# Performance work log

Hardware: AMD Instinct MI355X
Metric: run time of the kernel (lower is better)

The kernel has to match this reference:

```python
import jax, jax.numpy as jnp
import numpy as np

M, K, N = 8192, 4096, 4096  # tokens, in_features, out_features

def setup_inputs() -> dict:
    key = jax.random.key(0)
    k1, k2, k3 = jax.random.split(key, 3)
    x = jax.random.normal(k1, (M, K), dtype=jnp.float32)
    # kaiming_uniform_(a=sqrt(5)) on [out,in] -> uniform(-1/sqrt(in), 1/sqrt(in))
    bound = 1.0 / np.sqrt(K)
    weight = jax.random.uniform(k2, (N, K), dtype=jnp.float32, minval=-bound, maxval=bound)
    bias = jax.random.uniform(k3, (N,), dtype=jnp.float32, minval=-bound, maxval=bound)
    return {
        "x": x,
        "weight": weight,
        "bias": bias,
        "input_scale": jnp.float32(1.0),
        "weight_scale": jnp.float32(1.0),
    }


def reference(x, weight, bias, input_scale, weight_scale):
    # Quantize input and weight to fp8 e4m3 (per-tensor scale = 1.0 in module),
    # then dequant-matmul: out = (x_fp8 @ w_fp8^T) * scale_a * scale_b + bias,
    # matching torch._scaled_mm semantics with out_dtype=float32.
    x_fp8 = x.astype(jnp.float8_e4m3fn)
    w_fp8 = weight.astype(jnp.float8_e4m3fn)
    out = jnp.einsum(
        "mk,nk->mn",
        x_fp8.astype(jnp.float32),
        w_fp8.astype(jnp.float32),
    ) * (input_scale * weight_scale)
    return out + bias[None, :]
```

## Files before the change

kernel.cpp:

```cpp
#include <hip/hip_runtime.h>
#include <hip/hip_fp8.h>
#include <cstdint>

typedef float f32x4 __attribute__((ext_vector_type(4)));
typedef int i32x8 __attribute__((ext_vector_type(8)));
typedef long long i64;

static constexpr int Mdim = 8192;
static constexpr int Kdim = 4096;
static constexpr int Ndim = 4096;

static constexpr int BM = 256, BN = 256, BK = 128;
static constexpr int NT = Kdim / BK;
static constexpr int NWG_M = Mdim / BM;
static constexpr int NWG_N = Ndim / BN;
static constexpr int NWG = NWG_M * NWG_N;
static_assert(NT >= 4, "pipeline needs >=4 K-tiles");

__device__ __forceinline__ uint8_t f32_to_e4m3(float f) {
  return (uint8_t)__hip_cvt_float_to_fp8(f, __HIP_SATFINITE, __HIP_E4M3);
}

__global__ __launch_bounds__(256) void quant_fp8_kernel(
    const float* __restrict__ in, uint8_t* __restrict__ out, int n_vec16) {
  const int stride = gridDim.x * blockDim.x;
  for (int i = blockIdx.x * blockDim.x + threadIdx.x; i < n_vec16; i += stride) {
    const float4* src = reinterpret_cast<const float4*>(in) + (size_t)i * 4;
    float4 f0 = src[0], f1 = src[1], f2 = src[2], f3 = src[3];
    const float v[16] = {f0.x, f0.y, f0.z, f0.w, f1.x, f1.y, f1.z, f1.w,
                         f2.x, f2.y, f2.z, f2.w, f3.x, f3.y, f3.z, f3.w};
    union alignas(16) {
      uint32_t u[4];
      uint8_t b[16];
    } r;
#pragma unroll
    for (int j = 0; j < 16; ++j) r.b[j] = f32_to_e4m3(v[j]);
    reinterpret_cast<uint4*>(out)[i] = *reinterpret_cast<const uint4*>(r.u);
  }
}

__device__ __forceinline__ void gload_lds16(const uint8_t* g, uint8_t* l) {
  __builtin_amdgcn_global_load_lds(
      (const __attribute__((address_space(1))) void*)g,
      (__attribute__((address_space(3))) void*)l, 16, 0, 0);
}

__device__ __forceinline__ f32x4 mx_mfma(i32x8 a, i32x8 b, f32x4 c) {
  return __builtin_amdgcn_mfma_scale_f32_16x16x128_f8f6f4(
      a, b, c, 0, 0, 0, 0x7f7f7f7f, 0, 0x7f7f7f7f);
}

__global__ __launch_bounds__(512, 2) void gemm_fp8_mx_256(
    const uint8_t* __restrict__ Aq, const uint8_t* __restrict__ Bq,
    const float* __restrict__ bias, const float* __restrict__ sa,
    const float* __restrict__ sb, float* __restrict__ C) {
  __shared__ alignas(16) uint8_t sA[2][BM * BK];
  __shared__ alignas(16) uint8_t sB[2][BN * BK];

  int wg = (int)blockIdx.x;
  wg = (wg & 7) * (NWG / 8) + (wg >> 3);
  const int bm0 = (wg / NWG_N) * BM;
  const int bn0 = (wg % NWG_N) * BN;

  const int t = (int)threadIdx.x;
  const int lane = t & 63;
  const int wave = t >> 6;
  const int wm = wave >> 2;
  const int wn = wave & 3;

  const int srow = t >> 3;
  const int sc16 = (t & 7) ^ (srow & 7);
  const uint8_t* aBase = Aq + (size_t)(bm0 + srow) * Kdim + sc16 * 16;
  const uint8_t* bBase = Bq + (size_t)(bn0 + srow) * Kdim + sc16 * 16;
  const int ldsOff = t * 16;

  auto stageA = [&](int buf, int kt) {
    const size_t kb = (size_t)kt * BK;
#pragma unroll
    for (int i = 0; i < 4; ++i)
      gload_lds16(aBase + kb + (size_t)(i * 64) * Kdim,
                  &sA[buf][i * 8192 + ldsOff]);
  };
  auto stageB = [&](int buf, int kt) {
    const size_t kb = (size_t)kt * BK;
#pragma unroll
    for (int i = 0; i < 4; ++i)
      gload_lds16(bBase + kb + (size_t)(i * 64) * Kdim,
                  &sB[buf][i * 8192 + ldsOff]);
  };

  const int r7 = lane & 7;
  const int kg = (lane >> 4) * 2;
  const int off0 = (kg ^ r7) * 16;
  const int off1 = ((kg + 1) ^ r7) * 16;
  const int rbA = (wm * 128 + (lane & 15)) * BK;
  const int rbB = (wn * 64 + (lane & 15)) * BK;

  auto ldfrag = [&](const uint8_t* base) -> i32x8 {
    union {
      i32x8 v;
      int4 h[2];
    } u;
    u.h[0] = *reinterpret_cast<const int4*>(base + off0);
    u.h[1] = *reinterpret_cast<const int4*>(base + off1);
    return u.v;
  };

  f32x4 acc[8][4] = {};

  stageA(0, 0);
  stageB(0, 0);
  stageB(1, 1);
  asm volatile("s_waitcnt vmcnt(4)" ::: "memory");
  __builtin_amdgcn_s_barrier();

#pragma unroll 1
  for (int kt = 0; kt < NT; ++kt) {
    const int c = kt & 1;
    const int cn = c ^ 1;
    const uint8_t* A = &sA[c][0];
    const uint8_t* B = &sB[c][0];

    if (kt + 1 < NT) stageA(cn, kt + 1);

    i32x8 bf0 = ldfrag(B + rbB + 0 * 16 * BK);
    i32x8 bf1 = ldfrag(B + rbB + 1 * 16 * BK);
    i32x8 bf2 = ldfrag(B + rbB + 2 * 16 * BK);
    i32x8 bf3 = ldfrag(B + rbB + 3 * 16 * BK);
    i32x8 a0 = ldfrag(A + rbA + 0 * 16 * BK);
    i32x8 a1 = ldfrag(A + rbA + 1 * 16 * BK);
    i32x8 a2 = ldfrag(A + rbA + 2 * 16 * BK);
    i32x8 a3 = ldfrag(A + rbA + 3 * 16 * BK);

    __builtin_amdgcn_s_setprio(1);
    acc[0][0] = mx_mfma(a0, bf0, acc[0][0]);
    acc[0][1] = mx_mfma(a0, bf1, acc[0][1]);
    acc[0][2] = mx_mfma(a0, bf2, acc[0][2]);
    acc[0][3] = mx_mfma(a0, bf3, acc[0][3]);
    acc[1][0] = mx_mfma(a1, bf0, acc[1][0]);
    acc[1][1] = mx_mfma(a1, bf1, acc[1][1]);
    acc[1][2] = mx_mfma(a1, bf2, acc[1][2]);
    acc[1][3] = mx_mfma(a1, bf3, acc[1][3]);
    __builtin_amdgcn_s_setprio(0);

    __builtin_amdgcn_s_barrier();
    if (kt + 2 < NT) stageB(c, kt + 2);

    i32x8 a4 = ldfrag(A + rbA + 4 * 16 * BK);
    i32x8 a5 = ldfrag(A + rbA + 5 * 16 * BK);

    __builtin_amdgcn_s_setprio(1);
    acc[2][0] = mx_mfma(a2, bf0, acc[2][0]);
    acc[2][1] = mx_mfma(a2, bf1, acc[2][1]);
    acc[2][2] = mx_mfma(a2, bf2, acc[2][2]);
    acc[2][3] = mx_mfma(a2, bf3, acc[2][3]);
    acc[3][0] = mx_mfma(a3, bf0, acc[3][0]);
    acc[3][1] = mx_mfma(a3, bf1, acc[3][1]);
    acc[3][2] = mx_mfma(a3, bf2, acc[3][2]);
    acc[3][3] = mx_mfma(a3, bf3, acc[3][3]);
    __builtin_amdgcn_s_setprio(0);

    i32x8 a6 = ldfrag(A + rbA + 6 * 16 * BK);
    i32x8 a7 = ldfrag(A + rbA + 7 * 16 * BK);

    __builtin_amdgcn_s_setprio(1);
    acc[4][0] = mx_mfma(a4, bf0, acc[4][0]);
    acc[4][1] = mx_mfma(a4, bf1, acc[4][1]);
    acc[4][2] = mx_mfma(a4, bf2, acc[4][2]);
    acc[4][3] = mx_mfma(a4, bf3, acc[4][3]);
    acc[5][0] = mx_mfma(a5, bf0, acc[5][0]);
    acc[5][1] = mx_mfma(a5, bf1, acc[5][1]);
    acc[5][2] = mx_mfma(a5, bf2, acc[5][2]);
    acc[5][3] = mx_mfma(a5, bf3, acc[5][3]);
    __builtin_amdgcn_s_setprio(0);

    __builtin_amdgcn_s_setprio(1);
    acc[6][0] = mx_mfma(a6, bf0, acc[6][0]);
    acc[6][1] = mx_mfma(a6, bf1, acc[6][1]);
    acc[6][2] = mx_mfma(a6, bf2, acc[6][2]);
    acc[6][3] = mx_mfma(a6, bf3, acc[6][3]);
    acc[7][0] = mx_mfma(a7, bf0, acc[7][0]);
    acc[7][1] = mx_mfma(a7, bf1, acc[7][1]);
    acc[7][2] = mx_mfma(a7, bf2, acc[7][2]);
    acc[7][3] = mx_mfma(a7, bf3, acc[7][3]);
    __builtin_amdgcn_s_setprio(0);

    if (kt + 2 < NT) {
      asm volatile("s_waitcnt vmcnt(4)" ::: "memory");
    } else {
      asm volatile("s_waitcnt vmcnt(0)" ::: "memory");
    }
    __builtin_amdgcn_s_barrier();
  }

  const float scale = sa[0] * sb[0];
  const int orow0 = bm0 + wm * 128 + ((lane >> 4) << 2);
  const int ocol0 = bn0 + wn * 64 + (lane & 15);
#pragma unroll
  for (int n = 0; n < 4; ++n) {
    const int col = ocol0 + n * 16;
    const float bv = bias[col];
#pragma unroll
    for (int m = 0; m < 8; ++m) {
      const int row = orow0 + m * 16;
#pragma unroll
      for (int r = 0; r < 4; ++r)
        C[(size_t)(row + r) * Ndim + col] = acc[m][n][r] * scale + bv;
    }
  }
}

__device__ __forceinline__ void stage16_cvt(const float* g, uint8_t* l) {
  const float4* s = reinterpret_cast<const float4*>(g);
  float4 f0 = s[0], f1 = s[1], f2 = s[2], f3 = s[3];
  const float v[16] = {f0.x, f0.y, f0.z, f0.w, f1.x, f1.y, f1.z, f1.w,
                       f2.x, f2.y, f2.z, f2.w, f3.x, f3.y, f3.z, f3.w};
  union alignas(16) {
    uint32_t u[4];
    uint8_t b[16];
  } r;
#pragma unroll
  for (int j = 0; j < 16; ++j) r.b[j] = f32_to_e4m3(v[j]);
  *reinterpret_cast<uint4*>(l) = *reinterpret_cast<const uint4*>(r.u);
}

__global__ __launch_bounds__(256) void gemm_fp8_fused_kernel(
    const float* __restrict__ X, const float* __restrict__ W,
    const float* __restrict__ bias, const float* __restrict__ sa,
    const float* __restrict__ sb, float* __restrict__ C) {
  constexpr int FBM = 128, FBN = 128, FBK = 64;
  constexpr int FNWG_N = Ndim / FBN;
  __shared__ alignas(16) uint8_t As[FBM * FBK];
  __shared__ alignas(16) uint8_t Bs[FBN * FBK];

  int wg = (int)blockIdx.x;
  const int nwg = (Mdim / FBM) * FNWG_N;
  wg = (wg & 7) * (nwg / 8) + (wg >> 3);
  const int bm0 = (wg / FNWG_N) * FBM;
  const int bn0 = (wg % FNWG_N) * FBN;

  const int t = (int)threadIdx.x;
  const int lane = t & 63;
  const int wave = t >> 6;
  const int wm = wave >> 1, wn = wave & 1;

  const int c0 = t, c1 = t + 256;
  const int r0 = c0 >> 2, col0 = (c0 & 3) * 16;
  const int r1 = c1 >> 2, col1 = (c1 & 3) * 16;
  const float* xa0 = X + (size_t)(bm0 + r0) * Kdim + col0;
  const float* xa1 = X + (size_t)(bm0 + r1) * Kdim + col1;
  const float* wb0 = W + (size_t)(bn0 + r0) * Kdim + col0;
  const float* wb1 = W + (size_t)(bn0 + r1) * Kdim + col1;

  const int arow = (wm * 64 + (lane & 15)) * FBK;
  const int brow = (wn * 64 + (lane & 15)) * FBK;
  const int koff = (lane >> 4) * 8;

  f32x4 acc[4][4] = {};

  for (int kt = 0; kt < Kdim / FBK; ++kt) {
    const int kb = kt * FBK;
    stage16_cvt(xa0 + kb, As + c0 * 16);
    stage16_cvt(xa1 + kb, As + c1 * 16);
    stage16_cvt(wb0 + kb, Bs + c0 * 16);
    stage16_cvt(wb1 + kb, Bs + c1 * 16);
    __syncthreads();
#pragma unroll
    for (int kk = 0; kk < FBK / 32; ++kk) {
      i64 a[4], b[4];
#pragma unroll
      for (int m = 0; m < 4; ++m)
        a[m] = *reinterpret_cast<const i64*>(&As[arow + m * 16 * FBK + kk * 32 + koff]);
#pragma unroll
      for (int n = 0; n < 4; ++n)
        b[n] = *reinterpret_cast<const i64*>(&Bs[brow + n * 16 * FBK + kk * 32 + koff]);
#pragma unroll
      for (int m = 0; m < 4; ++m)
#pragma unroll
        for (int n = 0; n < 4; ++n)
          acc[m][n] = __builtin_amdgcn_mfma_f32_16x16x32_fp8_fp8(
              a[m], b[n], acc[m][n], 0, 0, 0);
    }
    __syncthreads();
  }

  const float scale = sa[0] * sb[0];
  const int orow0 = bm0 + wm * 64 + ((lane >> 4) << 2);
  const int ocol0 = bn0 + wn * 64 + (lane & 15);
#pragma unroll
  for (int n = 0; n < 4; ++n) {
    const int col = ocol0 + n * 16;
    const float bv = bias[col];
#pragma unroll
    for (int m = 0; m < 4; ++m) {
      const int row = orow0 + m * 16;
#pragma unroll
      for (int r = 0; r < 4; ++r)
        C[(size_t)(row + r) * Ndim + col] = acc[m][n][r] * scale + bv;
    }
  }
}

extern "C" void kernel_launch(void* const* d_in, const int* in_sizes, int n_in,
                              void* d_out, int out_size, void* d_ws, size_t ws_size,
                              hipStream_t stream) {
  const float* x = (const float*)d_in[0];
  const float* w = (const float*)d_in[1];
  const float* bias = (const float*)d_in[2];
  const float* s_in = (const float*)d_in[3];
  const float* s_w = (const float*)d_in[4];
  float* out = (float*)d_out;

  const size_t needA = (size_t)Mdim * Kdim;
  const size_t needB = (size_t)Ndim * Kdim;

  if (ws_size >= needA + needB) {
    uint8_t* Aq = (uint8_t*)d_ws;
    uint8_t* Bq = Aq + needA;
    quant_fp8_kernel<<<2048, 256, 0, stream>>>(x, Aq, (int)(needA / 16));
    quant_fp8_kernel<<<2048, 256, 0, stream>>>(w, Bq, (int)(needB / 16));
    gemm_fp8_mx_256<<<NWG, 512, 0, stream>>>(Aq, Bq, bias, s_in, s_w, out);
  } else {
    gemm_fp8_fused_kernel<<<(Mdim / 128) * (Ndim / 128), 256, 0, stream>>>(
        x, w, bias, s_in, s_w, out);
  }
}
```

Before: 200.8 us.

## Load B fragments directly from global memory and remap workgroups per XCD

The B tile is no longer staged through LDS. Each wave now loads its B MFMA fragments straight from global memory into registers every K-step, which halves LDS usage and removes the mid-loop barrier. The workgroup-to-tile mapping is also changed so that each XCD owns two N column blocks, letting those B rows stay hot in that XCD's L2. In exchange, B is read redundantly by waves that share it, each iteration now has global-load latency on its critical path, and the wait before the barrier becomes vmcnt(0), which shortens the prefetch window.

```diff
diff --git a/kernel.cpp b/kernel.cpp
--- a/kernel.cpp
+++ b/kernel.cpp
@@ -15,7 +15,6 @@
 static constexpr int NWG_M = Mdim / BM;
 static constexpr int NWG_N = Ndim / BN;
 static constexpr int NWG = NWG_M * NWG_N;
-static_assert(NT >= 4, "pipeline needs >=4 K-tiles");
 
 __device__ __forceinline__ uint8_t f32_to_e4m3(float f) {
   return (uint8_t)__hip_cvt_float_to_fp8(f, __HIP_SATFINITE, __HIP_E4M3);
@@ -50,17 +49,17 @@
       a, b, c, 0, 0, 0, 0x7f7f7f7f, 0, 0x7f7f7f7f);
 }
 
-__global__ __launch_bounds__(512, 2) void gemm_fp8_mx_256(
+__global__ __launch_bounds__(512, 2) void gemm_fp8_mx_bl2(
     const uint8_t* __restrict__ Aq, const uint8_t* __restrict__ Bq,
     const float* __restrict__ bias, const float* __restrict__ sa,
     const float* __restrict__ sb, float* __restrict__ C) {
   __shared__ alignas(16) uint8_t sA[2][BM * BK];
-  __shared__ alignas(16) uint8_t sB[2][BN * BK];
-
-  int wg = (int)blockIdx.x;
-  wg = (wg & 7) * (NWG / 8) + (wg >> 3);
-  const int bm0 = (wg / NWG_N) * BM;
-  const int bn0 = (wg % NWG_N) * BN;
+
+  const int wg = (int)blockIdx.x;
+  const int xcd = wg & 7;
+  const int within = wg >> 3;
+  const int bn0 = (xcd * 2 + (within >> 5)) * BN;
+  const int bm0 = (within & 31) * BM;
 
   const int t = (int)threadIdx.x;
   const int lane = t & 63;
@@ -71,7 +70,6 @@
   const int srow = t >> 3;
   const int sc16 = (t & 7) ^ (srow & 7);
   const uint8_t* aBase = Aq + (size_t)(bm0 + srow) * Kdim + sc16 * 16;
-  const uint8_t* bBase = Bq + (size_t)(bn0 + srow) * Kdim + sc16 * 16;
   const int ldsOff = t * 16;
 
   auto stageA = [&](int buf, int kt) {
@@ -80,13 +78,6 @@
     for (int i = 0; i < 4; ++i)
       gload_lds16(aBase + kb + (size_t)(i * 64) * Kdim,
                   &sA[buf][i * 8192 + ldsOff]);
-  };
-  auto stageB = [&](int buf, int kt) {
-    const size_t kb = (size_t)kt * BK;
-#pragma unroll
-    for (int i = 0; i < 4; ++i)
-      gload_lds16(bBase + kb + (size_t)(i * 64) * Kdim,
-                  &sB[buf][i * 8192 + ldsOff]);
   };
 
   const int r7 = lane & 7;
@@ -94,7 +85,6 @@
   const int off0 = (kg ^ r7) * 16;
   const int off1 = ((kg + 1) ^ r7) * 16;
   const int rbA = (wm * 128 + (lane & 15)) * BK;
-  const int rbB = (wn * 64 + (lane & 15)) * BK;
 
   auto ldfrag = [&](const uint8_t* base) -> i32x8 {
     union {
@@ -106,27 +96,38 @@
     return u.v;
   };
 
+  const uint8_t* bFrag =
+      Bq + (size_t)(bn0 + wn * 64 + (lane & 15)) * Kdim + ((lane >> 4) * 32);
+  auto ldb = [&](int n, size_t kb) -> i32x8 {
+    const uint8_t* p = bFrag + (size_t)(n * 16) * Kdim + kb;
+    union {
+      i32x8 v;
+      int4 h[2];
+    } u;
+    u.h[0] = *reinterpret_cast<const int4*>(p);
+    u.h[1] = *reinterpret_cast<const int4*>(p + 16);
+    return u.v;
+  };
+
   f32x4 acc[8][4] = {};
 
   stageA(0, 0);
-  stageB(0, 0);
-  stageB(1, 1);
-  asm volatile("s_waitcnt vmcnt(4)" ::: "memory");
+  asm volatile("s_waitcnt vmcnt(0)" ::: "memory");
   __builtin_amdgcn_s_barrier();
 
 #pragma unroll 1
   for (int kt = 0; kt < NT; ++kt) {
     const int c = kt & 1;
-    const int cn = c ^ 1;
     const uint8_t* A = &sA[c][0];
-    const uint8_t* B = &sB[c][0];
-
-    if (kt + 1 < NT) stageA(cn, kt + 1);
-
-    i32x8 bf0 = ldfrag(B + rbB + 0 * 16 * BK);
-    i32x8 bf1 = ldfrag(B + rbB + 1 * 16 * BK);
-    i32x8 bf2 = ldfrag(B + rbB + 2 * 16 * BK);
-    i32x8 bf3 = ldfrag(B + rbB + 3 * 16 * BK);
+    const size_t kb = (size_t)kt * BK;
+
+    i32x8 bf0 = ldb(0, kb);
+    i32x8 bf1 = ldb(1, kb);
+    i32x8 bf2 = ldb(2, kb);
+    i32x8 bf3 = ldb(3, kb);
+
+    if (kt + 1 < NT) stageA(c ^ 1, kt + 1);
+
     i32x8 a0 = ldfrag(A + rbA + 0 * 16 * BK);
     i32x8 a1 = ldfrag(A + rbA + 1 * 16 * BK);
     i32x8 a2 = ldfrag(A + rbA + 2 * 16 * BK);
@@ -143,9 +144,6 @@
     acc[1][3] = mx_mfma(a1, bf3, acc[1][3]);
     __builtin_amdgcn_s_setprio(0);
 
-    __builtin_amdgcn_s_barrier();
-    if (kt + 2 < NT) stageB(c, kt + 2);
-
     i32x8 a4 = ldfrag(A + rbA + 4 * 16 * BK);
     i32x8 a5 = ldfrag(A + rbA + 5 * 16 * BK);
 
@@ -185,11 +183,7 @@
     acc[7][3] = mx_mfma(a7, bf3, acc[7][3]);
     __builtin_amdgcn_s_setprio(0);
 
-    if (kt + 2 < NT) {
-      asm volatile("s_waitcnt vmcnt(4)" ::: "memory");
-    } else {
-      asm volatile("s_waitcnt vmcnt(0)" ::: "memory");
-    }
+    asm volatile("s_waitcnt vmcnt(0)" ::: "memory");
     __builtin_amdgcn_s_barrier();
   }
 
@@ -319,7 +313,7 @@
     uint8_t* Bq = Aq + needA;
     quant_fp8_kernel<<<2048, 256, 0, stream>>>(x, Aq, (int)(needA / 16));
     quant_fp8_kernel<<<2048, 256, 0, stream>>>(w, Bq, (int)(needB / 16));
-    gemm_fp8_mx_256<<<NWG, 512, 0, stream>>>(Aq, Bq, bias, s_in, s_w, out);
+    gemm_fp8_mx_bl2<<<NWG, 512, 0, stream>>>(Aq, Bq, bias, s_in, s_w, out);
   } else {
     gemm_fp8_fused_kernel<<<(Mdim / 128) * (Ndim / 128), 256, 0, stream>>>(
         x, w, bias, s_in, s_w, out);
```

After: 271.9 us. 35.4% more time.
